# Optimization experiments

Hardware: AMD Instinct MI355X
Metric: run time of the kernel (lower is better)

## Reference

```python
import jax, jax.numpy as jnp
import numpy as np

DIM = 1024
H = 16
HD = DIM // H          # head_dim = 64
SCALE = HD ** -0.5
LAMBDA_INIT = 0.1


def setup_inputs() -> dict:
    key = jax.random.key(0)
    ks = jax.random.split(key, 8)
    B, NQ, NKV = 4, 1024, 1024
    # xavier_uniform for linear weights; stored as (in, out) for x @ W
    def xavier(k, fan_in, fan_out):
        a = float(np.sqrt(6.0 / (fan_in + fan_out)))
        return jax.random.uniform(k, (fan_in, fan_out), jnp.float32, -a, a)
    return {
        "DriftData": jax.random.normal(ks[0], (B, NQ, DIM), jnp.float32),
        "OceanData": jax.random.normal(ks[1], (B, NKV, DIM), jnp.float32),
        "Wq": xavier(ks[2], DIM, 2 * DIM),
        "Wk": xavier(ks[3], DIM, 2 * DIM),
        "Wv": xavier(ks[4], DIM, DIM),
        "Wo": xavier(ks[5], DIM, DIM),
        "lambda_q1": jax.random.normal(ks[6], (H, HD), jnp.float32),
        "lambda_k1": jax.random.normal(jax.random.fold_in(ks[6], 1), (H, HD), jnp.float32),
        "lambda_q2": jax.random.normal(ks[7], (H, HD), jnp.float32),
        "lambda_k2": jax.random.normal(jax.random.fold_in(ks[7], 1), (H, HD), jnp.float32),
    }


def reference(DriftData, OceanData, Wq, Wk, Wv, Wo,
              lambda_q1, lambda_k1, lambda_q2, lambda_k2):
    B, NQ, dim = DriftData.shape
    NKV = OceanData.shape[1]
    # lambda scalar per head: exp(q1.k1) - exp(q2.k2) + lambda_init  -> (H,)
    lam = (jnp.exp(jnp.sum(lambda_q1 * lambda_k1, axis=-1))
           - jnp.exp(jnp.sum(lambda_q2 * lambda_k2, axis=-1)) + LAMBDA_INIT)
    # projections: Q,K -> 2*dim, V -> dim
    Q = (DriftData @ Wq).reshape(B, NQ, H, 2 * HD).transpose(0, 2, 1, 3)   # b h q 2hd
    K = (OceanData @ Wk).reshape(B, NKV, H, 2 * HD).transpose(0, 2, 1, 3)  # b h k 2hd
    V = (OceanData @ Wv).reshape(B, NKV, H, HD).transpose(0, 2, 1, 3)      # b h k hd
    Q1, Q2 = Q[..., :HD], Q[..., HD:]
    K1, K2 = K[..., :HD], K[..., HD:]
    A1 = jnp.einsum('bhqd,bhkd->bhqk', Q1, K1) * SCALE
    A2 = jnp.einsum('bhqd,bhkd->bhqk', Q2, K2) * SCALE
    att = jax.nn.softmax(A1, axis=-1) - lam[None, :, None, None] * jax.nn.softmax(A2, axis=-1)
    out = jnp.einsum('bhqk,bhkd->bhqd', att, V)            # b h q hd
    out = out.transpose(0, 2, 1, 3).reshape(B, NQ, dim)    # b q dim
    return out @ Wo
```

## Files before the change

### kernel.cpp

```cpp
#include <hip/hip_runtime.h>
#include <hip/hip_bf16.h>

typedef unsigned short u16;
typedef unsigned int u32;
typedef __attribute__((ext_vector_type(8))) short short8;
typedef __attribute__((ext_vector_type(4))) float f32x4;
typedef __attribute__((ext_vector_type(4))) u16 us4;

#define MFMA16(a,b,c) __builtin_amdgcn_mfma_f32_16x16x32_bf16(a,b,c,0,0,0)

__device__ __forceinline__ u16 f2b(float x){
  u32 u = __builtin_bit_cast(u32, x);
  u32 r = (u + 0x7fffu + ((u >> 16) & 1u)) >> 16;
  return (u16)r;
}
__device__ __forceinline__ u16 f2b_hw(float x){
  return __builtin_bit_cast(u16, __float2bfloat16(x));
}
__device__ __forceinline__ float ex2(float x){ return __builtin_amdgcn_exp2f(x); }

__device__ __forceinline__ void gll16(const u16* g, u16* l){
  __builtin_amdgcn_global_load_lds((const __attribute__((address_space(1))) u32*)g,
                                   (__attribute__((address_space(3))) u32*)l, 16, 0, 0);
}

__global__ __launch_bounds__(256) void k_prep(const float* __restrict__ Drift, const float* __restrict__ Ocean,
                                              const float* __restrict__ Wq, const float* __restrict__ Wk,
                                              const float* __restrict__ Wv, const float* __restrict__ Wo,
                                              u16* __restrict__ Xd, u16* __restrict__ Xo,
                                              u16* __restrict__ WqT, u16* __restrict__ WkvT,
                                              u16* __restrict__ WoT,
                                              const float* __restrict__ lq1, const float* __restrict__ lk1,
                                              const float* __restrict__ lq2, const float* __restrict__ lk2,
                                              float* __restrict__ lam){
  __shared__ float t[32][33];
  int bid = blockIdx.x;
  if (bid < 8192){
    const float* x = (bid < 4096) ? Drift : Ocean;
    u16* y = (bid < 4096) ? Xd : Xo;
    int i = (bid & 4095) * 256 + threadIdx.x;
    float4 v = reinterpret_cast<const float4*>(x)[i];
    us4 o; o.x = f2b(v.x); o.y = f2b(v.y); o.z = f2b(v.z); o.w = f2b(v.w);
    reinterpret_cast<us4*>(y)[i] = o;
    return;
  }
  int tt = bid - 8192;
  int z = tt >> 11;
  int bx = tt & 63, by = (tt & 2047) >> 6;
  const float* W; u16* WT; int N; float scale = 1.0f;
  if (z == 0){ W = Wq; WT = WqT; N = 2048; scale = 0.1803368867f; }
  else if (z == 1){ W = Wk; WT = WkvT; N = 2048; }
  else if (z == 2){ W = Wv; WT = WkvT + 2048*1024; N = 1024; }
  else { W = Wo; WT = WoT; N = 1024; }
  int n0 = bx * 32, k0 = by * 32;
  int tx = threadIdx.x & 31, ty = threadIdx.x >> 5;
  if (n0 < N){
    #pragma unroll
    for (int i = 0; i < 4; i++)
      t[ty + i*8][tx] = W[(size_t)(k0 + ty + i*8) * N + n0 + tx];
    __syncthreads();
    #pragma unroll
    for (int i = 0; i < 4; i++)
      WT[(size_t)(n0 + ty + i*8) * 1024 + k0 + tx] = f2b(t[tx][ty + i*8] * scale);
  }
  if (z == 3 && bx == 0 && by == 0 && threadIdx.x < 16){
    int h = threadIdx.x;
    float d1 = 0.f, d2 = 0.f;
    for (int i = 0; i < 64; i++){
      d1 += lq1[h*64 + i] * lk1[h*64 + i];
      d2 += lq2[h*64 + i] * lk2[h*64 + i];
    }
    lam[h] = expf(d1) - expf(d2) + 0.1f;
  }
}

__global__ __launch_bounds__(256) void k_transpose_v(const u16* __restrict__ KV, u16* __restrict__ VT){
  __shared__ u16 t[32][34];
  int kv0 = blockIdx.x * 32, d0 = blockIdx.y * 32, bh = blockIdx.z;
  int b = bh >> 4, h = bh & 15;
  int tx = threadIdx.x & 31, ty = threadIdx.x >> 5;
  #pragma unroll
  for (int i = 0; i < 4; i++)
    t[ty + i*8][tx] = KV[(size_t)(b*1024 + kv0 + ty + i*8) * 3072 + 2048 + h*64 + d0 + tx];
  __syncthreads();
  #pragma unroll
  for (int i = 0; i < 4; i++)
    VT[(size_t)bh * 65536 + (size_t)(d0 + ty + i*8) * 1024 + kv0 + tx] = t[tx][ty + i*8];
}

template<bool OUTF32>
__device__ __forceinline__ void gemm_body(const u16* __restrict__ A, const u16* __restrict__ B,
                                          void* __restrict__ C, int N, int m0, int n0,
                                          u16* As, u16* Bs){
  const int tid = threadIdx.x;
  const int wave = tid >> 6, lane = tid & 63;
  const int lr = lane & 15, lg = lane >> 4;
  const int wm = wave >> 1, wn = wave & 1;

  f32x4 acc[4][4];
  #pragma unroll
  for (int i = 0; i < 4; i++)
    #pragma unroll
    for (int j = 0; j < 4; j++){ f32x4 z = {0.f,0.f,0.f,0.f}; acc[i][j] = z; }

  const int srow = tid >> 3;
  const int skc  = tid & 7;

  for (int k0 = 0; k0 < 1024; k0 += 64){
    #pragma unroll
    for (int c = 0; c < 4; c++){
      int row = c*32 + srow;
      const u16* ga = A + (size_t)(m0 + row) * 1024 + k0 + ((skc ^ (row & 7)) << 3);
      gll16(ga, As + c*2048 + wave*512);
      const u16* gb = B + (size_t)(n0 + row) * 1024 + k0 + ((skc ^ (row & 7)) << 3);
      gll16(gb, Bs + c*2048 + wave*512);
    }
    __syncthreads();
    #pragma unroll
    for (int kc = 0; kc < 2; kc++){
      short8 af[4], bfr[4];
      #pragma unroll
      for (int mt = 0; mt < 4; mt++){
        int row = wm*64 + mt*16 + lr;
        af[mt] = *reinterpret_cast<const short8*>(As + row*64 + (((kc*4 + lg) ^ (row & 7)) << 3));
      }
      #pragma unroll
      for (int nt = 0; nt < 4; nt++){
        int rown = wn*64 + nt*16 + lr;
        bfr[nt] = *reinterpret_cast<const short8*>(Bs + rown*64 + (((kc*4 + lg) ^ (rown & 7)) << 3));
      }
      #pragma unroll
      for (int mt = 0; mt < 4; mt++)
        #pragma unroll
        for (int nt = 0; nt < 4; nt++)
          acc[mt][nt] = MFMA16(af[mt], bfr[nt], acc[mt][nt]);
    }
    __syncthreads();
  }
  #pragma unroll
  for (int mt = 0; mt < 4; mt++)
    #pragma unroll
    for (int nt = 0; nt < 4; nt++)
      #pragma unroll
      for (int r = 0; r < 4; r++){
        int row = m0 + wm*64 + mt*16 + lg*4 + r;
        int col = n0 + wn*64 + nt*16 + lr;
        if (OUTF32) ((float*)C)[(size_t)row * N + col] = acc[mt][nt][r];
        else        ((u16*)C)[(size_t)row * N + col] = f2b(acc[mt][nt][r]);
      }
}

__global__ __launch_bounds__(256) void k_gemm_proj(const u16* __restrict__ Xd, const u16* __restrict__ Xo,
                                                   const u16* __restrict__ WqT, const u16* __restrict__ WkvT,
                                                   u16* __restrict__ Qb, u16* __restrict__ KVb){
  __shared__ __align__(16) u16 As[128*64];
  __shared__ __align__(16) u16 Bs[128*64];
  int bid0 = blockIdx.x;
  int bid = (bid0 & 7) * 160 + (bid0 >> 3);
  if (bid < 512){
    gemm_body<false>(Xd, WqT, Qb, 2048, (bid >> 4) * 128, (bid & 15) * 128, As, Bs);
  } else {
    int t = bid - 512;
    gemm_body<false>(Xo, WkvT, KVb, 3072, (t / 24) * 128, (t % 24) * 128, As, Bs);
  }
}

__global__ __launch_bounds__(256) void k_gemm_out(const u16* __restrict__ A, const u16* __restrict__ B,
                                                  float* __restrict__ C){
  __shared__ __align__(16) u16 As[128*64];
  __shared__ __align__(16) u16 Bs[128*64];
  int bid = blockIdx.x;
  gemm_body<true>(A, B, C, 1024, (bid >> 3) * 128, (bid & 7) * 128, As, Bs);
}

__device__ __forceinline__ void softmax_t(f32x4 s[4], float& l, u16* pl, int lr, int lg){
  float sum = 0.f;
  #pragma unroll
  for (int nt = 0; nt < 4; nt++)
    #pragma unroll
    for (int r = 0; r < 4; r++){
      float p = ex2(s[nt][r]);
      s[nt][r] = p;
      sum += p;
    }
  sum += __shfl_xor(sum, 16);
  sum += __shfl_xor(sum, 32);
  l += sum;
  char* base = (char*)pl + lr * 128;
  const int swz = (lr & 7) << 4;
  #pragma unroll
  for (int nt = 0; nt < 4; nt++){
    us4 h;
    h.x = f2b_hw(s[nt][0]); h.y = f2b_hw(s[nt][1]);
    h.z = f2b_hw(s[nt][2]); h.w = f2b_hw(s[nt][3]);
    *reinterpret_cast<us4*>(base + ((nt*32 + lg*8) ^ swz)) = h;
  }
}

__global__ __launch_bounds__(512) void k_attn(const u16* __restrict__ Q, const u16* __restrict__ KVb,
                                              const u16* __restrict__ VT, const float* __restrict__ lam,
                                              u16* __restrict__ O){
  int bid = blockIdx.x;
  int logical = (bid & 7) * 32 + (bid >> 3);
  int qt2 = logical & 3, h = (logical >> 2) & 15, b = logical >> 6;
  const int tid = threadIdx.x, wave = tid >> 6, lane = tid & 63;
  const int lr = lane & 15, lg = lane >> 4;
  const int qb = qt2 * 256 + wave * 32;

  __shared__ __align__(16) u16 Ks[2][8192];
  __shared__ __align__(16) u16 Vs[2][4096];
  __shared__ __align__(16) u16 Pl[8][2][2][1024];

  const int srow = tid >> 4, schunk = tid & 15;
  const int vrow = tid >> 3, vchunk = tid & 7;
  const u16* Kg = KVb + (size_t)(b*1024 + srow) * 3072 + h*128 + ((schunk ^ (srow & 7)) << 3);
  const u16* Vg = VT + (size_t)(b*16 + h) * 65536 + (size_t)vrow * 1024 + ((vchunk ^ (vrow & 7)) << 3);

  short8 qf[2][2][2];
  #pragma unroll
  for (int qt = 0; qt < 2; qt++){
    const u16* Qp = Q + (size_t)(b*1024 + qb + qt*16 + lr) * 2048 + h*128 + lg*8;
    #pragma unroll
    for (int kc = 0; kc < 2; kc++){
      qf[0][qt][kc] = *reinterpret_cast<const short8*>(Qp + kc*32);
      qf[1][qt][kc] = *reinterpret_cast<const short8*>(Qp + 64 + kc*32);
    }
  }
  const float lamh = lam[h];

  f32x4 o[2][4][2];
  #pragma unroll
  for (int br = 0; br < 2; br++)
    #pragma unroll
    for (int nt = 0; nt < 4; nt++)
      #pragma unroll
      for (int qt = 0; qt < 2; qt++){ f32x4 z = {0.f,0.f,0.f,0.f}; o[br][nt][qt] = z; }
  float l[2][2] = {{0.f, 0.f}, {0.f, 0.f}};

  auto STAGE = [&](int buf, int kv0){
    #pragma unroll
    for (int i = 0; i < 2; i++)
      gll16(Kg + (size_t)(kv0 + i*32) * 3072, &Ks[buf][i*4096 + tid*8]);
    gll16(Vg + kv0, &Vs[buf][tid*8]);
  };

  STAGE(0, 0);
  __syncthreads();

  for (int t = 0; t < 16; t++){
    const int cur = t & 1;
    if (t < 15) STAGE(cur ^ 1, (t + 1) << 6);

    const u16* kbuf = &Ks[cur][0];
    const u16* vbuf = &Vs[cur][0];

    #pragma unroll
    for (int br = 0; br < 2; br++){
      short8 kf[4][2];
      #pragma unroll
      for (int nt = 0; nt < 4; nt++)
        #pragma unroll
        for (int kc = 0; kc < 2; kc++)
          kf[nt][kc] = *reinterpret_cast<const short8*>(
              kbuf + (nt*16 + lr)*128 + (((br*8 + kc*4 + lg) ^ (lr & 7)) << 3));
      #pragma unroll
      for (int qt = 0; qt < 2; qt++){
        f32x4 s[4];
        #pragma unroll
        for (int nt = 0; nt < 4; nt++){ f32x4 z = {0.f,0.f,0.f,0.f}; s[nt] = z; }
        __builtin_amdgcn_s_setprio(1);
        #pragma unroll
        for (int nt = 0; nt < 4; nt++)
          #pragma unroll
          for (int kc = 0; kc < 2; kc++)
            s[nt] = MFMA16(kf[nt][kc], qf[br][qt][kc], s[nt]);
        __builtin_amdgcn_s_setprio(0);
        softmax_t(s, l[br][qt], &Pl[wave][qt][br][0], lr, lg);
      }
    }

    const int swz = (lr & 7) << 4;
    __builtin_amdgcn_s_setprio(1);
    #pragma unroll
    for (int kc = 0; kc < 2; kc++){
      short8 pf[2][2];
      #pragma unroll
      for (int qt = 0; qt < 2; qt++)
        #pragma unroll
        for (int br = 0; br < 2; br++)
          pf[qt][br] = *reinterpret_cast<const short8*>(
              (char*)&Pl[wave][qt][br][0] + lr*128 + ((kc*64 + lg*16) ^ swz));
      #pragma unroll
      for (int nt = 0; nt < 4; nt++){
        short8 vf = *reinterpret_cast<const short8*>(
            vbuf + (nt*16 + lr)*64 + (((kc*4 + lg) ^ (lr & 7)) << 3));
        #pragma unroll
        for (int qt = 0; qt < 2; qt++){
          o[0][nt][qt] = MFMA16(vf, pf[qt][0], o[0][nt][qt]);
          o[1][nt][qt] = MFMA16(vf, pf[qt][1], o[1][nt][qt]);
        }
      }
    }
    __builtin_amdgcn_s_setprio(0);
    __syncthreads();
  }

  #pragma unroll
  for (int qt = 0; qt < 2; qt++){
    const float inv1 = 1.0f / l[0][qt];
    const float inv2 = lamh / l[1][qt];
    u16* Op = O + (size_t)(b*1024 + qb + qt*16 + lr) * 1024 + h*64;
    #pragma unroll
    for (int nt = 0; nt < 4; nt++){
      us4 hh;
      #pragma unroll
      for (int r = 0; r < 4; r++){
        float v = o[0][nt][qt][r] * inv1 - o[1][nt][qt][r] * inv2;
        ((u16*)&hh)[r] = f2b_hw(v);
      }
      *reinterpret_cast<us4*>(Op + nt*16 + lg*4) = hh;
    }
  }
}

extern "C" void kernel_launch(void* const* d_in, const int* in_sizes, int n_in,
                              void* d_out, int out_size, void* d_ws, size_t ws_size,
                              hipStream_t stream){
  const float* Drift = (const float*)d_in[0];
  const float* Ocean = (const float*)d_in[1];
  const float* Wq    = (const float*)d_in[2];
  const float* Wk    = (const float*)d_in[3];
  const float* Wv    = (const float*)d_in[4];
  const float* Wo    = (const float*)d_in[5];
  const float* lq1   = (const float*)d_in[6];
  const float* lk1   = (const float*)d_in[7];
  const float* lq2   = (const float*)d_in[8];
  const float* lk2   = (const float*)d_in[9];
  float* out = (float*)d_out;

  char* ws = (char*)d_ws;
  u16* Xd   = (u16*)(ws);
  u16* Xo   = (u16*)(ws + 8388608);
  u16* WqT  = (u16*)(ws + 16777216);
  u16* WkvT = (u16*)(ws + 20971520);
  u16* WoT  = (u16*)(ws + 27262976);
  u16* Qb   = (u16*)(ws + 29360128);
  u16* KVb  = (u16*)(ws + 46137344);
  u16* VTb  = (u16*)(ws + 71303168);
  u16* Ob   = (u16*)(ws + 79691776);
  float* lam = (float*)(ws + 88080384);

  k_prep<<<16384, 256, 0, stream>>>(Drift, Ocean, Wq, Wk, Wv, Wo, Xd, Xo,
                                    WqT, WkvT, WoT, lq1, lk1, lq2, lk2, lam);
  k_gemm_proj<<<1280, 256, 0, stream>>>(Xd, Xo, WqT, WkvT, Qb, KVb);
  k_transpose_v<<<dim3(32,2,64), 256, 0, stream>>>(KVb, VTb);
  k_attn<<<256, 512, 0, stream>>>(Qb, KVb, VTb, lam, Ob);
  k_gemm_out<<<256, 256, 0, stream>>>(Ob, WoT, out);
}
```

Measured before the change: 143.2 us.

## Split attention branches across waves and triple-buffer K/V with fine-grained waits

Each wave now handles a single softmax branch (Q1K1 or Q2K2) for 64 query rows, where before each wave handled both branches for 32 rows. The two branch results are merged at the end through LDS, with the second branch stored in bf16. K/V staging moves from double to triple buffering, using explicit vmcnt waits and raw barriers so loads run two tiles ahead. A new XOR swizzle is applied to the P scratch layout. This is meant to halve the K-fragment LDS reads per wave and overlap global loads better. The cost is more LDS, an extra rounding of the branch-2 result to bf16, and a final barrier.

```diff
diff --git a/kernel.cpp b/kernel.cpp
--- a/kernel.cpp
+++ b/kernel.cpp
@@ -18,6 +18,7 @@
   return __builtin_bit_cast(u16, __float2bfloat16(x));
 }
 __device__ __forceinline__ float ex2(float x){ return __builtin_amdgcn_exp2f(x); }
+__device__ __forceinline__ float b2f(u16 v){ return __builtin_bit_cast(float, ((u32)v) << 16); }
 
 __device__ __forceinline__ void gll16(const u16* g, u16* l){
   __builtin_amdgcn_global_load_lds((const __attribute__((address_space(1))) u32*)g,
@@ -173,7 +174,7 @@
   gemm_body<true>(A, B, C, 1024, (bid >> 3) * 128, (bid & 7) * 128, As, Bs);
 }
 
-__device__ __forceinline__ void softmax_t(f32x4 s[4], float& l, u16* pl, int lr, int lg){
+__device__ __forceinline__ void softmax_t(f32x4 s[4], float& l, u16* pl, int lr, int lg, int swzv){
   float sum = 0.f;
   #pragma unroll
   for (int nt = 0; nt < 4; nt++)
@@ -187,13 +188,12 @@
   sum += __shfl_xor(sum, 32);
   l += sum;
   char* base = (char*)pl + lr * 128;
-  const int swz = (lr & 7) << 4;
   #pragma unroll
   for (int nt = 0; nt < 4; nt++){
     us4 h;
     h.x = f2b_hw(s[nt][0]); h.y = f2b_hw(s[nt][1]);
     h.z = f2b_hw(s[nt][2]); h.w = f2b_hw(s[nt][3]);
-    *reinterpret_cast<us4*>(base + ((nt*32 + lg*8) ^ swz)) = h;
+    *reinterpret_cast<us4*>(base + ((nt*32 + lg*8) ^ (swzv << 4))) = h;
   }
 }
 
@@ -205,37 +205,33 @@
   int qt2 = logical & 3, h = (logical >> 2) & 15, b = logical >> 6;
   const int tid = threadIdx.x, wave = tid >> 6, lane = tid & 63;
   const int lr = lane & 15, lg = lane >> 4;
-  const int qb = qt2 * 256 + wave * 32;
-
-  __shared__ __align__(16) u16 Ks[2][8192];
-  __shared__ __align__(16) u16 Vs[2][4096];
-  __shared__ __align__(16) u16 Pl[8][2][2][1024];
+  const int br = wave >> 2, wq = wave & 3;
+  const int swzv = (lr ^ (lr >> 3)) & 7;
+
+  __shared__ __align__(16) u16 Ks[3][8192];
+  __shared__ __align__(16) u16 Vs[3][4096];
+  __shared__ __align__(16) u16 Pl[8][4][1024];
 
   const int srow = tid >> 4, schunk = tid & 15;
   const int vrow = tid >> 3, vchunk = tid & 7;
   const u16* Kg = KVb + (size_t)(b*1024 + srow) * 3072 + h*128 + ((schunk ^ (srow & 7)) << 3);
   const u16* Vg = VT + (size_t)(b*16 + h) * 65536 + (size_t)vrow * 1024 + ((vchunk ^ (vrow & 7)) << 3);
 
-  short8 qf[2][2][2];
-  #pragma unroll
-  for (int qt = 0; qt < 2; qt++){
-    const u16* Qp = Q + (size_t)(b*1024 + qb + qt*16 + lr) * 2048 + h*128 + lg*8;
-    #pragma unroll
-    for (int kc = 0; kc < 2; kc++){
-      qf[0][qt][kc] = *reinterpret_cast<const short8*>(Qp + kc*32);
-      qf[1][qt][kc] = *reinterpret_cast<const short8*>(Qp + 64 + kc*32);
-    }
+  short8 qf[4][2];
+  #pragma unroll
+  for (int qt = 0; qt < 4; qt++){
+    const u16* Qp = Q + (size_t)(b*1024 + qt2*256 + wq*64 + qt*16 + lr) * 2048 + h*128 + br*64 + lg*8;
+    qf[qt][0] = *reinterpret_cast<const short8*>(Qp);
+    qf[qt][1] = *reinterpret_cast<const short8*>(Qp + 32);
   }
   const float lamh = lam[h];
 
-  f32x4 o[2][4][2];
-  #pragma unroll
-  for (int br = 0; br < 2; br++)
-    #pragma unroll
-    for (int nt = 0; nt < 4; nt++)
-      #pragma unroll
-      for (int qt = 0; qt < 2; qt++){ f32x4 z = {0.f,0.f,0.f,0.f}; o[br][nt][qt] = z; }
-  float l[2][2] = {{0.f, 0.f}, {0.f, 0.f}};
+  f32x4 o[4][4];
+  #pragma unroll
+  for (int nt = 0; nt < 4; nt++)
+    #pragma unroll
+    for (int qt = 0; qt < 4; qt++){ f32x4 z = {0.f,0.f,0.f,0.f}; o[nt][qt] = z; }
+  float l[4] = {0.f, 0.f, 0.f, 0.f};
 
   auto STAGE = [&](int buf, int kv0){
     #pragma unroll
@@ -245,80 +241,106 @@
   };
 
   STAGE(0, 0);
-  __syncthreads();
+  STAGE(1, 64);
+  asm volatile("s_waitcnt vmcnt(3)" ::: "memory");
+  __builtin_amdgcn_s_barrier();
+  __builtin_amdgcn_sched_barrier(0);
+
+  u16* Plw = &Pl[wave][0][0];
 
   for (int t = 0; t < 16; t++){
-    const int cur = t & 1;
-    if (t < 15) STAGE(cur ^ 1, (t + 1) << 6);
+    const int cur = t % 3;
+    if (t <= 13) STAGE((t + 2) % 3, (t + 2) << 6);
 
     const u16* kbuf = &Ks[cur][0];
     const u16* vbuf = &Vs[cur][0];
 
-    #pragma unroll
-    for (int br = 0; br < 2; br++){
-      short8 kf[4][2];
+    short8 kf[4][2];
+    #pragma unroll
+    for (int nt = 0; nt < 4; nt++)
+      #pragma unroll
+      for (int kc = 0; kc < 2; kc++)
+        kf[nt][kc] = *reinterpret_cast<const short8*>(
+            kbuf + (nt*16 + lr)*128 + (((br*8 + kc*4 + lg) ^ (lr & 7)) << 3));
+    #pragma unroll
+    for (int qt = 0; qt < 4; qt++){
+      f32x4 s[4];
+      #pragma unroll
+      for (int nt = 0; nt < 4; nt++){ f32x4 z = {0.f,0.f,0.f,0.f}; s[nt] = z; }
+      __builtin_amdgcn_s_setprio(1);
       #pragma unroll
       for (int nt = 0; nt < 4; nt++)
         #pragma unroll
         for (int kc = 0; kc < 2; kc++)
-          kf[nt][kc] = *reinterpret_cast<const short8*>(
-              kbuf + (nt*16 + lr)*128 + (((br*8 + kc*4 + lg) ^ (lr & 7)) << 3));
-      #pragma unroll
-      for (int qt = 0; qt < 2; qt++){
-        f32x4 s[4];
-        #pragma unroll
-        for (int nt = 0; nt < 4; nt++){ f32x4 z = {0.f,0.f,0.f,0.f}; s[nt] = z; }
-        __builtin_amdgcn_s_setprio(1);
-        #pragma unroll
-        for (int nt = 0; nt < 4; nt++)
-          #pragma unroll
-          for (int kc = 0; kc < 2; kc++)
-            s[nt] = MFMA16(kf[nt][kc], qf[br][qt][kc], s[nt]);
-        __builtin_amdgcn_s_setprio(0);
-        softmax_t(s, l[br][qt], &Pl[wave][qt][br][0], lr, lg);
-      }
-    }
-
-    const int swz = (lr & 7) << 4;
-    __builtin_amdgcn_s_setprio(1);
+          s[nt] = MFMA16(kf[nt][kc], qf[qt][kc], s[nt]);
+      __builtin_amdgcn_s_setprio(0);
+      softmax_t(s, l[qt], Plw + qt*1024, lr, lg, swzv);
+    }
+
     #pragma unroll
     for (int kc = 0; kc < 2; kc++){
-      short8 pf[2][2];
-      #pragma unroll
-      for (int qt = 0; qt < 2; qt++)
-        #pragma unroll
-        for (int br = 0; br < 2; br++)
-          pf[qt][br] = *reinterpret_cast<const short8*>(
-              (char*)&Pl[wave][qt][br][0] + lr*128 + ((kc*64 + lg*16) ^ swz));
+      short8 pf[4];
+      #pragma unroll
+      for (int qt = 0; qt < 4; qt++)
+        pf[qt] = *reinterpret_cast<const short8*>(
+            (char*)(Plw + qt*1024) + lr*128 + ((kc*64 + lg*16) ^ (swzv << 4)));
+      __builtin_amdgcn_s_setprio(1);
       #pragma unroll
       for (int nt = 0; nt < 4; nt++){
         short8 vf = *reinterpret_cast<const short8*>(
             vbuf + (nt*16 + lr)*64 + (((kc*4 + lg) ^ (lr & 7)) << 3));
         #pragma unroll
-        for (int qt = 0; qt < 2; qt++){
-          o[0][nt][qt] = MFMA16(vf, pf[qt][0], o[0][nt][qt]);
-          o[1][nt][qt] = MFMA16(vf, pf[qt][1], o[1][nt][qt]);
+        for (int qt = 0; qt < 4; qt++)
+          o[nt][qt] = MFMA16(vf, pf[qt], o[nt][qt]);
+      }
+      __builtin_amdgcn_s_setprio(0);
+    }
+
+    if (t <= 13){
+      asm volatile("s_waitcnt vmcnt(3)" ::: "memory");
+      __builtin_amdgcn_s_barrier();
+      __builtin_amdgcn_sched_barrier(0);
+    } else if (t == 14){
+      asm volatile("s_waitcnt vmcnt(0)" ::: "memory");
+      __builtin_amdgcn_s_barrier();
+      __builtin_amdgcn_sched_barrier(0);
+    }
+  }
+
+  if (br == 1){
+    #pragma unroll
+    for (int qt = 0; qt < 4; qt++){
+      const float inv2 = lamh / l[qt];
+      char* base = (char*)(Plw + qt*1024) + lr * 128;
+      #pragma unroll
+      for (int nt = 0; nt < 4; nt++){
+        us4 hh;
+        #pragma unroll
+        for (int r = 0; r < 4; r++)
+          ((u16*)&hh)[r] = f2b_hw(o[nt][qt][r] * inv2);
+        *reinterpret_cast<us4*>(base + ((nt*32 + lg*8) ^ (swzv << 4))) = hh;
+      }
+    }
+  }
+  __syncthreads();
+  if (br == 0){
+    u16* Px = &Pl[wave + 4][0][0];
+    #pragma unroll
+    for (int qt = 0; qt < 4; qt++){
+      const float inv1 = 1.0f / l[qt];
+      char* base = (char*)(Px + qt*1024) + lr * 128;
+      u16* Op = O + (size_t)(b*1024 + qt2*256 + wq*64 + qt*16 + lr) * 1024 + h*64;
+      #pragma unroll
+      for (int nt = 0; nt < 4; nt++){
+        us4 x = *reinterpret_cast<const us4*>(base + ((nt*32 + lg*8) ^ (swzv << 4)));
+        us4 hh;
+        #pragma unroll
+        for (int r = 0; r < 4; r++){
+          float v = o[nt][qt][r] * inv1 - b2f(((const u16*)&x)[r]);
+          ((u16*)&hh)[r] = f2b_hw(v);
         }
-      }
-    }
-    __builtin_amdgcn_s_setprio(0);
-    __syncthreads();
-  }
-
-  #pragma unroll
-  for (int qt = 0; qt < 2; qt++){
-    const float inv1 = 1.0f / l[0][qt];
-    const float inv2 = lamh / l[1][qt];
-    u16* Op = O + (size_t)(b*1024 + qb + qt*16 + lr) * 1024 + h*64;
-    #pragma unroll
-    for (int nt = 0; nt < 4; nt++){
-      us4 hh;
-      #pragma unroll
-      for (int r = 0; r < 4; r++){
-        float v = o[0][nt][qt][r] * inv1 - o[1][nt][qt][r] * inv2;
-        ((u16*)&hh)[r] = f2b_hw(v);
-      }
-      *reinterpret_cast<us4*>(Op + nt*16 + lg*4) = hh;
+        *reinterpret_cast<us4*>(Op + nt*16 + lg*4) = hh;
+      }
     }
   }
 }
```

After: 141.6 us (median of 2 runs). No clear change (-1.1%).
